# Kernel tuning notes

Hardware: AMD Instinct MI355X
Metric: run time of the kernel (lower is better)

## Reference

```python
import jax, jax.numpy as jnp
import numpy as np

N = 100000      # nodes
E = 1600000     # edges
IN_DIM = 128
OUT_DIM = 128
H = 8           # num_heads
D = OUT_DIM // H  # per-head dim = 16
L = 2           # num_layers
NEG_SLOPE = 0.1


def setup_inputs() -> dict:
    key = jax.random.key(0)
    ks = jax.random.split(key, 12)
    features = jax.random.normal(ks[0], (N, IN_DIM), dtype=jnp.float32)
    src = jax.random.randint(ks[1], (E,), 0, N, dtype=jnp.int32)
    dst = jax.random.randint(ks[2], (E,), 0, N, dtype=jnp.int32)
    w = jax.random.uniform(ks[3], (E,), dtype=jnp.float32)
    # per-layer params: fc weight [in, H*D], attn_left/right [H, D]
    s = 1.0 / np.sqrt(IN_DIM)
    W1 = jax.random.uniform(ks[4], (IN_DIM, H * D), minval=-s, maxval=s, dtype=jnp.float32)
    al1 = jax.random.normal(ks[5], (H, D), dtype=jnp.float32) * 0.1
    ar1 = jax.random.normal(ks[6], (H, D), dtype=jnp.float32) * 0.1
    W2 = jax.random.uniform(ks[7], (OUT_DIM, H * D), minval=-s, maxval=s, dtype=jnp.float32)
    al2 = jax.random.normal(ks[8], (H, D), dtype=jnp.float32) * 0.1
    ar2 = jax.random.normal(ks[9], (H, D), dtype=jnp.float32) * 0.1
    so = 1.0 / np.sqrt(L * OUT_DIM)
    Wm = jax.random.uniform(ks[10], (L * OUT_DIM, OUT_DIM), minval=-so, maxval=so, dtype=jnp.float32)
    bm = jax.random.uniform(ks[11], (OUT_DIM,), minval=-so, maxval=so, dtype=jnp.float32)
    return {"features": features, "src": src, "dst": dst, "w": w,
            "W1": W1, "al1": al1, "ar1": ar1, "W2": W2, "al2": al2, "ar2": ar2,
            "Wm": Wm, "bm": bm}


def gat_layer(x, src, dst, w, W, al, ar):
    # x: [N, in_dim] -> ft: [N, H, D]
    ft = (x @ W).reshape(N, H, D)
    el = jnp.einsum('nhd,hd->nh', ft, al)  # [N, H]
    er = jnp.einsum('nhd,hd->nh', ft, ar)  # [N, H]
    # edge-wise u_add_v + leaky_relu, scaled by edge weight w
    e = jax.nn.leaky_relu(el[src] + er[dst], negative_slope=NEG_SLOPE)  # [E, H]
    e = w[:, None] * e
    # edge_softmax over incoming edges of each dst node (numerically stable)
    m = jax.ops.segment_max(e, dst, num_segments=N)  # [N, H]
    m = jnp.where(jnp.isfinite(m), m, 0.0)           # empty segments -> 0
    ex = jnp.exp(e - m[dst])
    s = jax.ops.segment_sum(ex, dst, num_segments=N)  # [N, H] (>0 wherever indexed)
    a = ex / s[dst]                                   # [E, H]
    # u_mul_e + sum aggregation
    msg = ft[src] * a[:, :, None]                     # [E, H, D]
    out = jax.ops.segment_sum(msg, dst, num_segments=N)  # [N, H, D]
    out = jax.nn.relu(out)
    return out.reshape(N, H * D)  # concat heads


def reference(features, src, dst, w, W1, al1, ar1, W2, al2, ar2, Wm, bm):
    x1 = gat_layer(features, src, dst, w, W1, al1, ar1)
    x2 = gat_layer(x1, src, dst, w, W2, al2, ar2)
    h = jnp.concatenate([x1, x2], axis=-1)  # [N, L*OUT_DIM]
    return h @ Wm + bm                       # [N, OUT_DIM]
```

## Files before the change

### kernel.cpp

```cpp
#include <hip/hip_runtime.h>
#include <hip/hip_bf16.h>

#define NEG_SLOPE 0.1f
#define EPB 4096
#define BINSH 9
#define DMAX 256

typedef __attribute__((ext_vector_type(8))) short bf16x8;
typedef __attribute__((ext_vector_type(4))) float f32x4;

__device__ __forceinline__ float bflo(unsigned u) { return __uint_as_float(u << 16); }
__device__ __forceinline__ float bfhi(unsigned u) { return __uint_as_float(u & 0xffff0000u); }
__device__ __forceinline__ unsigned short f2bf(float f) {
    __hip_bfloat16 h = __float2bfloat16(f);
    unsigned short r;
    __builtin_memcpy(&r, &h, 2);
    return r;
}

__global__ __launch_bounds__(256) void binhist_k(const int* __restrict__ dst,
                                                 int* __restrict__ bin_counts, int E,
                                                 const float* __restrict__ W1,
                                                 const float* __restrict__ W2,
                                                 const float* __restrict__ Wm,
                                                 unsigned short* __restrict__ Wt1,
                                                 unsigned short* __restrict__ Wt2,
                                                 unsigned short* __restrict__ Wtm) {
    __shared__ int cnt[256];
    int t = threadIdx.x;
    cnt[t] = 0;
    __syncthreads();
    int base = blockIdx.x * EPB;
    if (base + EPB <= E) {
        const int4* d4 = (const int4*)(dst + base);
        #pragma unroll
        for (int i = 0; i < 4; ++i) {
            int4 v = d4[i * 256 + t];
            atomicAdd(&cnt[v.x >> BINSH], 1);
            atomicAdd(&cnt[v.y >> BINSH], 1);
            atomicAdd(&cnt[v.z >> BINSH], 1);
            atomicAdd(&cnt[v.w >> BINSH], 1);
        }
    } else {
        for (int i = 0; i < 4; ++i) {
            int j0 = base + (i * 256 + t) * 4;
            #pragma unroll
            for (int c = 0; c < 4; ++c)
                if (j0 + c < E) atomicAdd(&cnt[dst[j0 + c] >> BINSH], 1);
        }
    }
    int id = blockIdx.x * 256 + t;
    if (id < 16384) {
        int k = id >> 7, c = id & 127;
        Wt1[c * 128 + k] = f2bf(W1[id]);
    } else if (id < 32768) {
        int e = id - 16384; int k = e >> 7, c = e & 127;
        Wt2[c * 128 + k] = f2bf(W2[e]);
    } else if (id < 65536) {
        int e = id - 32768;
        int k = e >> 7, c = e & 127;
        Wtm[c * 256 + k] = f2bf(Wm[e]);
    }
    __syncthreads();
    if (cnt[t]) atomicAdd(&bin_counts[t], cnt[t]);
}

__global__ __launch_bounds__(256) void scan256_k(const int* __restrict__ bin_counts,
                                                 int* __restrict__ binoffs,
                                                 int* __restrict__ gcur, int nbins) {
    __shared__ int sbuf[256];
    int t = threadIdx.x;
    int c = (t < nbins) ? bin_counts[t] : 0;
    sbuf[t] = c;
    __syncthreads();
    for (int off = 1; off < 256; off <<= 1) {
        int u = (t >= off) ? sbuf[t - off] : 0;
        __syncthreads();
        sbuf[t] += u;
        __syncthreads();
    }
    int ex = sbuf[t] - c;
    binoffs[t] = ex;
    if (t == 255) binoffs[256] = ex + c;
    gcur[t] = ex;
}

__global__ __launch_bounds__(256) void binify_k(const int* __restrict__ src,
                                                const int* __restrict__ dst,
                                                const float* __restrict__ w,
                                                int* __restrict__ gcur,
                                                int2* __restrict__ tmp, int E) {
    __shared__ int cnt[256];
    __shared__ int basearr[256];
    int t = threadIdx.x;
    cnt[t] = 0;
    __syncthreads();
    int base = blockIdx.x * EPB;
    int es[16], ed[16], ew[16];
    bool va[16];
    if (base + EPB <= E) {
        const int4* s4 = (const int4*)(src + base);
        const int4* d4 = (const int4*)(dst + base);
        const int4* w4 = (const int4*)(w + base);
        #pragma unroll
        for (int i = 0; i < 4; ++i) {
            int slot = i * 256 + t;
            int4 sv = s4[slot]; int4 dv = d4[slot]; int4 wv = w4[slot];
            es[i*4+0]=sv.x; es[i*4+1]=sv.y; es[i*4+2]=sv.z; es[i*4+3]=sv.w;
            ed[i*4+0]=dv.x; ed[i*4+1]=dv.y; ed[i*4+2]=dv.z; ed[i*4+3]=dv.w;
            ew[i*4+0]=wv.x; ew[i*4+1]=wv.y; ew[i*4+2]=wv.z; ew[i*4+3]=wv.w;
            va[i*4+0]=va[i*4+1]=va[i*4+2]=va[i*4+3]=true;
        }
    } else {
        #pragma unroll
        for (int i = 0; i < 4; ++i) {
            #pragma unroll
            for (int c = 0; c < 4; ++c) {
                int j = base + (i * 256 + t) * 4 + c;
                bool v = j < E;
                va[i*4+c] = v;
                es[i*4+c] = v ? src[j] : 0;
                ed[i*4+c] = v ? dst[j] : 0;
                ew[i*4+c] = v ? __float_as_int(w[j]) : 0;
            }
        }
    }
    #pragma unroll
    for (int i = 0; i < 16; ++i)
        if (va[i]) atomicAdd(&cnt[ed[i] >> BINSH], 1);
    __syncthreads();
    int c = cnt[t];
    basearr[t] = c ? atomicAdd(&gcur[t], c) : 0;
    __syncthreads();
    cnt[t] = 0;
    __syncthreads();
    #pragma unroll
    for (int i = 0; i < 16; ++i) {
        if (va[i]) {
            int b = ed[i] >> BINSH;
            int pos = atomicAdd(&cnt[b], 1);
            tmp[basearr[b] + pos] = make_int2(es[i] | ((ed[i] & 511) << 17), ew[i]);
        }
    }
}

__global__ __launch_bounds__(256) void binfin_k(const int2* __restrict__ tmp,
                                                const int* __restrict__ binoffs,
                                                int* __restrict__ offs,
                                                int2* __restrict__ snw,
                                                int* __restrict__ dhist, int N, int E) {
    __shared__ int ncnt[512];
    __shared__ int noff[512];
    __shared__ int sbuf[256];
    __shared__ int dh[DMAX];
    int b = blockIdx.x, t = threadIdx.x;
    int lo = b << BINSH;
    int hi = min(lo + 512, N);
    int ebeg = binoffs[b], eend = binoffs[b + 1];
    ncnt[t] = 0; ncnt[t + 256] = 0; dh[t] = 0;
    __syncthreads();
    for (int j = ebeg + t; j < eend; j += 256)
        atomicAdd(&ncnt[(unsigned)tmp[j].x >> 17], 1);
    __syncthreads();
    int a0 = ncnt[2 * t], a1 = ncnt[2 * t + 1];
    sbuf[t] = a0 + a1;
    __syncthreads();
    for (int off = 1; off < 256; off <<= 1) {
        int u = (t >= off) ? sbuf[t - off] : 0;
        __syncthreads();
        sbuf[t] += u;
        __syncthreads();
    }
    int ex = sbuf[t] - (a0 + a1);
    noff[2 * t] = ex;
    noff[2 * t + 1] = ex + a0;
    if (lo + 2 * t < hi) {
        offs[lo + 2 * t] = ebeg + ex;
        atomicAdd(&dh[min(a0, DMAX - 1)], 1);
    }
    if (lo + 2 * t + 1 < hi) {
        offs[lo + 2 * t + 1] = ebeg + ex + a0;
        atomicAdd(&dh[min(a1, DMAX - 1)], 1);
    }
    if (b == 0 && t == 0) offs[N] = E;
    ncnt[t] = 0; ncnt[t + 256] = 0;
    __syncthreads();
    if (dh[t]) atomicAdd(&dhist[t], dh[t]);
    for (int j = ebeg + t; j < eend; j += 256) {
        int2 e = tmp[j];
        int idx = (unsigned)e.x >> 17;
        int pos = atomicAdd(&ncnt[idx], 1);
        snw[ebeg + noff[idx] + pos] = make_int2(e.x & 0x1ffff, e.y);
    }
}

__global__ __launch_bounds__(256) void degscan_k(const int* __restrict__ dhist,
                                                 int* __restrict__ dcur) {
    __shared__ int buf[DMAX];
    int t = threadIdx.x;
    int v = dhist[t];
    buf[t] = v;
    __syncthreads();
    for (int off = 1; off < DMAX; off <<= 1) {
        int u = (t >= off) ? buf[t - off] : 0;
        __syncthreads();
        buf[t] += u;
        __syncthreads();
    }
    dcur[t] = buf[t] - v;
}

__global__ __launch_bounds__(256) void degscat_k(const int* __restrict__ offs,
                                                 int* __restrict__ dcur,
                                                 int* __restrict__ perm, int N) {
    __shared__ int cnt[DMAX];
    __shared__ int basea[DMAX];
    int t = threadIdx.x;
    cnt[t] = 0;
    __syncthreads();
    int n = blockIdx.x * 256 + t;
    int d = -1;
    if (n < N) {
        d = min(offs[n + 1] - offs[n], DMAX - 1);
        atomicAdd(&cnt[d], 1);
    }
    __syncthreads();
    int c = cnt[t];
    basea[t] = c ? atomicAdd(&dcur[t], c) : 0;
    __syncthreads();
    cnt[t] = 0;
    __syncthreads();
    if (n < N) {
        int pos = atomicAdd(&cnt[d], 1);
        perm[basea[d] + pos] = n;
    }
}

template<int K, bool A_F32, bool BIAS, bool OUT_BF16>
__global__ __launch_bounds__(256) void gemm_mfma(const void* __restrict__ A0v,
                                                 const void* __restrict__ A1v,
                                                 const unsigned short* __restrict__ Wt,
                                                 const float* __restrict__ bias,
                                                 void* __restrict__ Cv, int M) {
    __shared__ __align__(16) unsigned short At[128 * 128];
    __shared__ __align__(16) unsigned short Bt[128 * 128];
    const int t = threadIdx.x;
    const int lane = t & 63;
    const int wv = t >> 6;
    const int m0 = blockIdx.x * 128;
    const int l15 = lane & 15;
    const int l4 = lane >> 4;

    f32x4 acc[2][8];
    #pragma unroll
    for (int r = 0; r < 2; ++r)
        #pragma unroll
        for (int c = 0; c < 8; ++c) acc[r][c] = (f32x4){0.f, 0.f, 0.f, 0.f};

    const int srow = t >> 4;
    const int scol = (t & 15) * 8;

    for (int k0 = 0; k0 < K; k0 += 128) {
        const int chunk = k0 >> 7;
        #pragma unroll
        for (int p = 0; p < 8; ++p) {
            int row = p * 16 + srow;
            int gm = m0 + row;
            uint4 pk = make_uint4(0, 0, 0, 0);
            if (A_F32) {
                const float* Ap = (const float*)(chunk ? A1v : A0v);
                float4 f0 = make_float4(0.f,0.f,0.f,0.f), f1 = f0;
                if (gm < M) {
                    f0 = *(const float4*)(Ap + (size_t)gm * 128 + scol);
                    f1 = *(const float4*)(Ap + (size_t)gm * 128 + scol + 4);
                }
                pk.x = f2bf(f0.x) | ((unsigned)f2bf(f0.y) << 16);
                pk.y = f2bf(f0.z) | ((unsigned)f2bf(f0.w) << 16);
                pk.z = f2bf(f1.x) | ((unsigned)f2bf(f1.y) << 16);
                pk.w = f2bf(f1.z) | ((unsigned)f2bf(f1.w) << 16);
            } else {
                const unsigned short* Ap = (const unsigned short*)(chunk ? A1v : A0v);
                if (gm < M) pk = *(const uint4*)(Ap + (size_t)gm * 128 + scol);
            }
            int byte = (row * 256 + scol * 2) ^ ((row & 7) << 4);
            *(uint4*)((char*)At + byte) = pk;
        }
        #pragma unroll
        for (int p = 0; p < 8; ++p) {
            int row = p * 16 + srow;
            uint4 pk = *(const uint4*)(Wt + (size_t)row * K + k0 + scol);
            int byte = (row * 256 + scol * 2) ^ ((row & 7) << 4);
            *(uint4*)((char*)Bt + byte) = pk;
        }
        __syncthreads();
        #pragma unroll
        for (int ks = 0; ks < 4; ++ks) {
            int kb = ks * 32 + l4 * 8;
            bf16x8 af[2], bfv[8];
            #pragma unroll
            for (int r = 0; r < 2; ++r) {
                int row = wv * 32 + r * 16 + l15;
                int byte = (row * 256 + kb * 2) ^ ((row & 7) << 4);
                af[r] = *(const bf16x8*)((char*)At + byte);
            }
            #pragma unroll
            for (int c = 0; c < 8; ++c) {
                int col = c * 16 + l15;
                int byte = (col * 256 + kb * 2) ^ ((col & 7) << 4);
                bfv[c] = *(const bf16x8*)((char*)Bt + byte);
            }
            #pragma unroll
            for (int r = 0; r < 2; ++r)
                #pragma unroll
                for (int c = 0; c < 8; ++c)
                    acc[r][c] = __builtin_amdgcn_mfma_f32_16x16x32_bf16(af[r], bfv[c], acc[r][c], 0, 0, 0);
        }
        __syncthreads();
    }
    float bb[8];
    if (BIAS) {
        #pragma unroll
        for (int c = 0; c < 8; ++c) bb[c] = bias[c * 16 + l15];
    }
    #pragma unroll
    for (int r = 0; r < 2; ++r) {
        #pragma unroll
        for (int q = 0; q < 4; ++q) {
            int row = m0 + wv * 32 + r * 16 + l4 * 4 + q;
            if (row < M) {
                #pragma unroll
                for (int c = 0; c < 8; ++c) {
                    int col = c * 16 + l15;
                    float v = acc[r][c][q];
                    if (BIAS) v += bb[c];
                    if (OUT_BF16) ((unsigned short*)Cv)[(size_t)row * 128 + col] = f2bf(v);
                    else          ((float*)Cv)[(size_t)row * 128 + col] = v;
                }
            }
        }
    }
}

__global__ __launch_bounds__(256) void agg_k(const __hip_bfloat16* __restrict__ ftb,
                                             const int2* __restrict__ snw,
                                             const int* __restrict__ offs,
                                             const int* __restrict__ perm,
                                             const float* __restrict__ AL,
                                             const float* __restrict__ AR,
                                             unsigned short* __restrict__ out, int n) {
    int tid = threadIdx.x;
    int gl = tid & 15;
    int hd = gl >> 1;
    unsigned gl16 = (unsigned)(gl * 16);
    int idx = blockIdx.x * 16 + (tid >> 4);
    bool valid = idx < n;
    int node = valid ? perm[idx] : 0;
    int beg = 0, deg = 0;
    if (valid) { beg = offs[node]; deg = offs[node + 1] - beg; }
    const char* fb = (const char*)ftb;

    float alf[8], arf[8];
    {
        const float* ap = AL + hd * 16 + (gl & 1) * 8;
        const float* rp = AR + hd * 16 + (gl & 1) * 8;
        #pragma unroll
        for (int d = 0; d < 8; ++d) { alf[d] = ap[d]; arf[d] = rp[d]; }
    }

    float er_h;
    {
        uint4 mu = *(const uint4*)(fb + ((unsigned)node << 8) + gl16);
        float ep = arf[0] * bflo(mu.x) + arf[1] * bfhi(mu.x)
                 + arf[2] * bflo(mu.y) + arf[3] * bfhi(mu.y)
                 + arf[4] * bflo(mu.z) + arf[5] * bfhi(mu.z)
                 + arf[6] * bflo(mu.w) + arf[7] * bfhi(mu.w);
        er_h = ep + __shfl_xor(ep, 1);
    }

    float acc[8];
    #pragma unroll
    for (int k = 0; k < 8; ++k) acc[k] = 0.f;
    float s = 0.f;

    for (int j0 = 0; j0 < deg; j0 += 8) {
        uint4 rv[8];
        float wv8[8];
        #pragma unroll
        for (int q = 0; q < 8; ++q) {
            int j = j0 + q;
            bool act = j < deg;
            int2 p2 = snw[act ? beg + j : 0];
            wv8[q] = act ? __int_as_float(p2.y) : 0.f;
            unsigned ad = act ? (((unsigned)p2.x << 8) + gl16) : gl16;
            rv[q] = *(const uint4*)(fb + ad);
        }
        #pragma unroll
        for (int q = 0; q < 8; ++q) {
            float ep = alf[0] * bflo(rv[q].x) + alf[1] * bfhi(rv[q].x)
                     + alf[2] * bflo(rv[q].y) + alf[3] * bfhi(rv[q].y)
                     + alf[4] * bflo(rv[q].z) + alf[5] * bfhi(rv[q].z)
                     + alf[6] * bflo(rv[q].w) + alf[7] * bfhi(rv[q].w);
            float el_h = ep + __shfl_xor(ep, 1);
            float tt = el_h + er_h;
            tt = tt > 0.f ? tt : NEG_SLOPE * tt;
            float p = __expf(tt * wv8[q]);
            p = (j0 + q < deg) ? p : 0.f;
            s += p;
            acc[0] += p * bflo(rv[q].x); acc[1] += p * bfhi(rv[q].x);
            acc[2] += p * bflo(rv[q].y); acc[3] += p * bfhi(rv[q].y);
            acc[4] += p * bflo(rv[q].z); acc[5] += p * bfhi(rv[q].z);
            acc[6] += p * bflo(rv[q].w); acc[7] += p * bfhi(rv[q].w);
        }
    }

    if (valid) {
        float sinv = s > 0.f ? 1.f / s : 0.f;
        float o[8];
        #pragma unroll
        for (int k = 0; k < 8; ++k) o[k] = fmaxf(acc[k] * sinv, 0.f);
        uint4 pk;
        pk.x = f2bf(o[0]) | ((unsigned)f2bf(o[1]) << 16);
        pk.y = f2bf(o[2]) | ((unsigned)f2bf(o[3]) << 16);
        pk.z = f2bf(o[4]) | ((unsigned)f2bf(o[5]) << 16);
        pk.w = f2bf(o[6]) | ((unsigned)f2bf(o[7]) << 16);
        *(uint4*)((char*)out + ((size_t)node << 8) + gl16) = pk;
    }
}

extern "C" void kernel_launch(void* const* d_in, const int* in_sizes, int n_in,
                              void* d_out, int out_size, void* d_ws, size_t ws_size,
                              hipStream_t stream) {
    const float* features = (const float*)d_in[0];
    const int*   src      = (const int*)d_in[1];
    const int*   dst      = (const int*)d_in[2];
    const float* w        = (const float*)d_in[3];
    const float* W1       = (const float*)d_in[4];
    const float* al1      = (const float*)d_in[5];
    const float* ar1      = (const float*)d_in[6];
    const float* W2       = (const float*)d_in[7];
    const float* al2      = (const float*)d_in[8];
    const float* ar2      = (const float*)d_in[9];
    const float* Wm       = (const float*)d_in[10];
    const float* bm       = (const float*)d_in[11];
    float* out = (float*)d_out;

    const int N = in_sizes[0] / 128;
    const int E = in_sizes[1];

    char* ws = (char*)d_ws;
    unsigned short* ftb = (unsigned short*)ws;            ws += (size_t)N * 128 * 2;
    unsigned short* x1b = (unsigned short*)ws;            ws += (size_t)N * 128 * 2;
    unsigned short* x2b = (unsigned short*)ws;            ws += (size_t)N * 128 * 2;
    unsigned short* Wt1 = (unsigned short*)ws;            ws += (size_t)128 * 128 * 2;
    unsigned short* Wt2 = (unsigned short*)ws;            ws += (size_t)128 * 128 * 2;
    unsigned short* Wtm = (unsigned short*)ws;            ws += (size_t)128 * 256 * 2;
    int* offs      = (int*)ws;                            ws += (size_t)(N + 4) * 4;
    int* bin_counts= (int*)ws;                            ws += 256 * 4;
    int* binoffs   = (int*)ws;                            ws += 260 * 4;
    int* gcur      = (int*)ws;                            ws += 256 * 4;
    int* dhist     = (int*)ws;                            ws += DMAX * 4;
    int* dcur      = (int*)ws;                            ws += DMAX * 4;
    int* perm      = (int*)ws;                            ws += (size_t)N * 4;
    int2* snw      = (int2*)ws;                           ws += (size_t)E * 8;
    int2* tmp      = (int2*)ws;                           ws += (size_t)E * 8;

    hipMemsetAsync(bin_counts, 0, 256 * sizeof(int), stream);
    hipMemsetAsync(dhist, 0, DMAX * sizeof(int), stream);

    const int nbins = (N + 511) >> BINSH;
    const int nblk_e = (E + EPB - 1) / EPB;
    const int nblk_n = (N + 255) / 256;

    binhist_k<<<nblk_e, 256, 0, stream>>>(dst, bin_counts, E, W1, W2, Wm, Wt1, Wt2, Wtm);
    scan256_k<<<1, 256, 0, stream>>>(bin_counts, binoffs, gcur, nbins);
    binify_k<<<nblk_e, 256, 0, stream>>>(src, dst, w, gcur, tmp, E);
    binfin_k<<<nbins, 256, 0, stream>>>(tmp, binoffs, offs, snw, dhist, N, E);
    degscan_k<<<1, 256, 0, stream>>>(dhist, dcur);
    degscat_k<<<nblk_n, 256, 0, stream>>>(offs, dcur, perm, N);

    int gemm_grid = (N + 127) / 128;
    int agg_grid = (N + 15) / 16;

    gemm_mfma<128, true, false, true><<<gemm_grid, 256, 0, stream>>>(features, nullptr, Wt1, nullptr, ftb, N);
    agg_k<<<agg_grid, 256, 0, stream>>>((const __hip_bfloat16*)ftb, snw, offs, perm, al1, ar1, x1b, N);

    gemm_mfma<128, false, false, true><<<gemm_grid, 256, 0, stream>>>(x1b, nullptr, Wt2, nullptr, ftb, N);
    agg_k<<<agg_grid, 256, 0, stream>>>((const __hip_bfloat16*)ftb, snw, offs, perm, al2, ar2, x2b, N);

    gemm_mfma<256, false, true, false><<<gemm_grid, 256, 0, stream>>>(x1b, x2b, Wtm, bm, out, N);
}
```

Baseline: 282.7 us.

## Load GEMM operands directly from global and stage bf16 output through LDS

The MFMA GEMM no longer stages A and W tiles in shared memory. Each wave loads its A fragments and W fragments straight from global memory into registers and runs the MFMAs without block barriers, and rows past M are clamped to M-1 instead of zero-filled. For bf16 output, the accumulator tile is written into a padded LDS buffer and then copied out as coalesced 16-byte row stores. This removes LDS round-trips and syncs in the main loop but relies on cache for W reuse across waves and issues less coalesced global reads for A.

```diff
diff --git a/kernel.cpp b/kernel.cpp
--- a/kernel.cpp
+++ b/kernel.cpp
@@ -242,8 +242,7 @@
                                                  const unsigned short* __restrict__ Wt,
                                                  const float* __restrict__ bias,
                                                  void* __restrict__ Cv, int M) {
-    __shared__ __align__(16) unsigned short At[128 * 128];
-    __shared__ __align__(16) unsigned short Bt[128 * 128];
+    __shared__ __align__(16) unsigned short Cs[128][136];
     const int t = threadIdx.x;
     const int lane = t & 63;
     const int wv = t >> 6;
@@ -257,87 +256,86 @@
         #pragma unroll
         for (int c = 0; c < 8; ++c) acc[r][c] = (f32x4){0.f, 0.f, 0.f, 0.f};
 
-    const int srow = t >> 4;
-    const int scol = (t & 15) * 8;
-
-    for (int k0 = 0; k0 < K; k0 += 128) {
-        const int chunk = k0 >> 7;
-        #pragma unroll
-        for (int p = 0; p < 8; ++p) {
-            int row = p * 16 + srow;
-            int gm = m0 + row;
-            uint4 pk = make_uint4(0, 0, 0, 0);
+    int rowA[2];
+    rowA[0] = min(m0 + wv * 32 + l15, M - 1);
+    rowA[1] = min(m0 + wv * 32 + 16 + l15, M - 1);
+
+    #pragma unroll
+    for (int ks = 0; ks < K / 32; ++ks) {
+        const int kb = ks * 32 + l4 * 8;
+        bf16x8 af[2], bfv[8];
+        #pragma unroll
+        for (int r = 0; r < 2; ++r) {
             if (A_F32) {
-                const float* Ap = (const float*)(chunk ? A1v : A0v);
-                float4 f0 = make_float4(0.f,0.f,0.f,0.f), f1 = f0;
-                if (gm < M) {
-                    f0 = *(const float4*)(Ap + (size_t)gm * 128 + scol);
-                    f1 = *(const float4*)(Ap + (size_t)gm * 128 + scol + 4);
-                }
-                pk.x = f2bf(f0.x) | ((unsigned)f2bf(f0.y) << 16);
-                pk.y = f2bf(f0.z) | ((unsigned)f2bf(f0.w) << 16);
-                pk.z = f2bf(f1.x) | ((unsigned)f2bf(f1.y) << 16);
-                pk.w = f2bf(f1.z) | ((unsigned)f2bf(f1.w) << 16);
+                const float* Ap = (const float*)A0v;
+                float4 f0 = *(const float4*)(Ap + (size_t)rowA[r] * 128 + kb);
+                float4 f1 = *(const float4*)(Ap + (size_t)rowA[r] * 128 + kb + 4);
+                union { bf16x8 v; unsigned u[4]; } cv;
+                cv.u[0] = f2bf(f0.x) | ((unsigned)f2bf(f0.y) << 16);
+                cv.u[1] = f2bf(f0.z) | ((unsigned)f2bf(f0.w) << 16);
+                cv.u[2] = f2bf(f1.x) | ((unsigned)f2bf(f1.y) << 16);
+                cv.u[3] = f2bf(f1.z) | ((unsigned)f2bf(f1.w) << 16);
+                af[r] = cv.v;
             } else {
-                const unsigned short* Ap = (const unsigned short*)(chunk ? A1v : A0v);
-                if (gm < M) pk = *(const uint4*)(Ap + (size_t)gm * 128 + scol);
+                const unsigned short* Ap = (const unsigned short*)((K == 256 && ks >= 4) ? A1v : A0v);
+                int kl = (K == 256 && ks >= 4) ? kb - 128 : kb;
+                af[r] = *(const bf16x8*)(Ap + (size_t)rowA[r] * 128 + kl);
             }
-            int byte = (row * 256 + scol * 2) ^ ((row & 7) << 4);
-            *(uint4*)((char*)At + byte) = pk;
-        }
-        #pragma unroll
-        for (int p = 0; p < 8; ++p) {
-            int row = p * 16 + srow;
-            uint4 pk = *(const uint4*)(Wt + (size_t)row * K + k0 + scol);
-            int byte = (row * 256 + scol * 2) ^ ((row & 7) << 4);
-            *(uint4*)((char*)Bt + byte) = pk;
-        }
-        __syncthreads();
-        #pragma unroll
-        for (int ks = 0; ks < 4; ++ks) {
-            int kb = ks * 32 + l4 * 8;
-            bf16x8 af[2], bfv[8];
-            #pragma unroll
-            for (int r = 0; r < 2; ++r) {
-                int row = wv * 32 + r * 16 + l15;
-                int byte = (row * 256 + kb * 2) ^ ((row & 7) << 4);
-                af[r] = *(const bf16x8*)((char*)At + byte);
-            }
-            #pragma unroll
-            for (int c = 0; c < 8; ++c) {
-                int col = c * 16 + l15;
-                int byte = (col * 256 + kb * 2) ^ ((col & 7) << 4);
-                bfv[c] = *(const bf16x8*)((char*)Bt + byte);
-            }
-            #pragma unroll
-            for (int r = 0; r < 2; ++r)
-                #pragma unroll
-                for (int c = 0; c < 8; ++c)
-                    acc[r][c] = __builtin_amdgcn_mfma_f32_16x16x32_bf16(af[r], bfv[c], acc[r][c], 0, 0, 0);
-        }
-        __syncthreads();
-    }
+        }
+        #pragma unroll
+        for (int c = 0; c < 8; ++c)
+            bfv[c] = *(const bf16x8*)(Wt + (size_t)(c * 16 + l15) * K + kb);
+        #pragma unroll
+        for (int r = 0; r < 2; ++r)
+            #pragma unroll
+            for (int c = 0; c < 8; ++c)
+                acc[r][c] = __builtin_amdgcn_mfma_f32_16x16x32_bf16(af[r], bfv[c], acc[r][c], 0, 0, 0);
+    }
+
     float bb[8];
     if (BIAS) {
         #pragma unroll
         for (int c = 0; c < 8; ++c) bb[c] = bias[c * 16 + l15];
     }
-    #pragma unroll
-    for (int r = 0; r < 2; ++r) {
-        #pragma unroll
-        for (int q = 0; q < 4; ++q) {
-            int row = m0 + wv * 32 + r * 16 + l4 * 4 + q;
-            if (row < M) {
+
+    if (OUT_BF16) {
+        #pragma unroll
+        for (int r = 0; r < 2; ++r)
+            #pragma unroll
+            for (int q = 0; q < 4; ++q) {
+                int row = wv * 32 + r * 16 + l4 * 4 + q;
                 #pragma unroll
                 for (int c = 0; c < 8; ++c) {
-                    int col = c * 16 + l15;
                     float v = acc[r][c][q];
                     if (BIAS) v += bb[c];
-                    if (OUT_BF16) ((unsigned short*)Cv)[(size_t)row * 128 + col] = f2bf(v);
-                    else          ((float*)Cv)[(size_t)row * 128 + col] = v;
+                    Cs[row][c * 16 + l15] = f2bf(v);
                 }
             }
-        }
+        __syncthreads();
+        int row = t >> 1, half = t & 1;
+        int gm = m0 + row;
+        if (gm < M) {
+            const char* sp = (const char*)Cs + (size_t)row * 272 + half * 128;
+            char* dp = (char*)Cv + (size_t)gm * 256 + half * 128;
+            #pragma unroll
+            for (int i = 0; i < 8; ++i)
+                *(uint4*)(dp + i * 16) = *(const uint4*)(sp + i * 16);
+        }
+    } else {
+        #pragma unroll
+        for (int r = 0; r < 2; ++r)
+            #pragma unroll
+            for (int q = 0; q < 4; ++q) {
+                int row = m0 + wv * 32 + r * 16 + l4 * 4 + q;
+                if (row < M) {
+                    #pragma unroll
+                    for (int c = 0; c < 8; ++c) {
+                        float v = acc[r][c][q];
+                        if (BIAS) v += bb[c];
+                        ((float*)Cv)[(size_t)row * 128 + c * 16 + l15] = v;
+                    }
+                }
+            }
     }
 }
 
```

New measurement: 328.6 us. 1.16x slower.
